# Performance work log

Measured on AMD Instinct MI355X. Metric: run time of the kernel, lower is better.

The kernel has to match this reference:

```python
import jax, jax.numpy as jnp
import numpy as np

HID = 64      # hidden_dim
HEADS = 4     # attention heads
CH = HID // HEADS  # 16 per-head channels
EDIM = 6      # edge_dim
NEG = 0.2     # leaky_relu negative slope


def _glorot(key, shape):
    fan_in, fan_out = shape[0], shape[-1]
    s = np.sqrt(6.0 / (fan_in + fan_out)).astype(np.float32)
    return jax.random.uniform(key, shape, jnp.float32, -s, s)


def setup_inputs() -> dict:
    key = jax.random.key(0)
    ks = iter(jax.random.split(key, 48))
    N, E, T = 100000, 1200000, 20000
    inp = {
        "x": jax.random.normal(next(ks), (N, 7), jnp.float32),
        "pos": jax.random.normal(next(ks), (N, 3), jnp.float32),
        "node_type": jax.random.randint(next(ks), (N,), 0, 2),
        "edge_index": jax.random.randint(next(ks), (2, E), 0, N),
        "edge_attr": jax.random.normal(next(ks), (E, EDIM), jnp.float32),
        "num_tracks": T,
        "hidden_state": jax.random.normal(next(ks), (T, HID), jnp.float32),
        # params
        "type_emb": jax.random.normal(next(ks), (2, 8), jnp.float32),
        "enc_W1": _glorot(next(ks), (18, HID)), "enc_b1": jnp.zeros((HID,), jnp.float32),
        "enc_W2": _glorot(next(ks), (HID, HID)), "enc_b2": jnp.zeros((HID,), jnp.float32),
        "gru_Wi": _glorot(next(ks), (HID, 3 * HID)), "gru_bi": jnp.zeros((3 * HID,), jnp.float32),
        "gru_Wh": _glorot(next(ks), (HID, 3 * HID)), "gru_bh": jnp.zeros((3 * HID,), jnp.float32),
        "dec_W1": _glorot(next(ks), (HID, HID)), "dec_b1": jnp.zeros((HID,), jnp.float32),
        "dec_W2": _glorot(next(ks), (HID, 7)), "dec_b2": jnp.zeros((7,), jnp.float32),
    }
    for g in ("g1", "g2"):
        inp[g + "_Wl"] = _glorot(next(ks), (HID, HID))
        inp[g + "_bl"] = jnp.zeros((HID,), jnp.float32)
        inp[g + "_Wr"] = _glorot(next(ks), (HID, HID))
        inp[g + "_br"] = jnp.zeros((HID,), jnp.float32)
        inp[g + "_We"] = _glorot(next(ks), (EDIM, HID))
        inp[g + "_att"] = _glorot(next(ks), (HEADS, CH))
        inp[g + "_bias"] = jnp.zeros((HID,), jnp.float32)
    return inp


def _segment_softmax(e, seg, n):
    m = jax.ops.segment_max(e, seg, num_segments=n)
    m = jnp.where(jnp.isfinite(m), m, 0.0)
    ex = jnp.exp(e - m[seg])
    s = jax.ops.segment_sum(ex, seg, num_segments=n)
    return ex / (s[seg] + 1e-16)


def _gatv2(h, src, dst, eattr, Wl, bl, Wr, br, We, att, bias):
    N = h.shape[0]
    xl = (h @ Wl + bl).reshape(N, HEADS, CH)
    xr = (h @ Wr + br).reshape(N, HEADS, CH)
    ea = (eattr @ We).reshape(-1, HEADS, CH)
    g = jax.nn.leaky_relu(xl[src] + xr[dst] + ea, NEG)      # [E, H, C]
    e = jnp.einsum('ehc,hc->eh', g, att)                     # [E, H]
    alpha = _segment_softmax(e, dst, N)                      # [E, H]
    msg = xl[src] * alpha[..., None]                         # [E, H, C]
    out = jax.ops.segment_sum(msg, dst, num_segments=N)
    return out.reshape(N, HID) + bias, alpha


def reference(x, pos, node_type, edge_index, edge_attr, num_tracks, hidden_state,
              type_emb, enc_W1, enc_b1, enc_W2, enc_b2,
              g1_Wl, g1_bl, g1_Wr, g1_br, g1_We, g1_att, g1_bias,
              g2_Wl, g2_bl, g2_Wr, g2_br, g2_We, g2_att, g2_bias,
              gru_Wi, gru_bi, gru_Wh, gru_bh,
              dec_W1, dec_b1, dec_W2, dec_b2):
    N = x.shape[0]
    h = jnp.concatenate([x, pos, type_emb[node_type]], axis=-1)
    h = jax.nn.relu(h @ enc_W1 + enc_b1) @ enc_W2 + enc_b2

    # PyG GATv2Conv: add self loops, edge_attr fill_value='mean' (mean of incoming edges)
    src, dst = edge_index[0], edge_index[1]
    deg = jax.ops.segment_sum(jnp.ones(src.shape[0], jnp.float32), dst, num_segments=N)
    loop_attr = jax.ops.segment_sum(edge_attr, dst, num_segments=N) / jnp.maximum(deg, 1.0)[:, None]
    ar = jnp.arange(N)
    src_a = jnp.concatenate([src, ar])
    dst_a = jnp.concatenate([dst, ar])
    eattr_a = jnp.concatenate([edge_attr, loop_attr], axis=0)

    h1, a1 = _gatv2(h, src_a, dst_a, eattr_a, g1_Wl, g1_bl, g1_Wr, g1_br, g1_We, g1_att, g1_bias)
    h1 = jax.nn.relu(h1)
    h2, a2 = _gatv2(h1, src_a, dst_a, eattr_a, g2_Wl, g2_bl, g2_Wr, g2_br, g2_We, g2_att, g2_bias)

    # GRUCell on the first num_tracks nodes
    ht = h2[:num_tracks]
    gi = ht @ gru_Wi + gru_bi
    gh = hidden_state @ gru_Wh + gru_bh
    r = jax.nn.sigmoid(gi[:, :HID] + gh[:, :HID])
    z = jax.nn.sigmoid(gi[:, HID:2 * HID] + gh[:, HID:2 * HID])
    n = jnp.tanh(gi[:, 2 * HID:] + r * gh[:, 2 * HID:])
    new_tracks = (1.0 - z) * n + z * hidden_state

    new_full = jnp.concatenate([new_tracks, h2[num_tracks:]], axis=0)
    out = jax.nn.relu(new_full @ dec_W1 + dec_b1) @ dec_W2 + dec_b2  # [N, 7]
    final = out.at[:, :3].set(pos + out[:, :3])
    final = final.at[:, 3:6].set(x[:, :3] + out[:, 3:6])
    return final, new_full, a1, a2
```

## Files before the change

kernel.cpp:

```cpp
#include <hip/hip_runtime.h>

#define NEG 0.2f
#define SCHUNK 1024
typedef unsigned short u16;

__device__ __forceinline__ float sigmoidf_(float v){ return 1.f/(1.f+__expf(-v)); }
__device__ __forceinline__ int rfl_(int v){ return __builtin_amdgcn_readfirstlane(v); }
__device__ __forceinline__ float bf2f_(unsigned u){ return __uint_as_float(u<<16); }
__device__ __forceinline__ u16 f2bf_(float f){
  unsigned u = __float_as_uint(f);
  u += 0x7FFFu + ((u>>16)&1u);
  return (u16)(u>>16);
}
template<int C>
__device__ __forceinline__ float dppadd_(float p){
  int r = __builtin_amdgcn_update_dpp(0, __float_as_int(p), C, 0xF, 0xF, true);
  return p + __int_as_float(r);
}
__device__ __forceinline__ float dppsum16_(float p){
  p = dppadd_<0x121>(p);
  p = dppadd_<0x122>(p);
  p = dppadd_<0x124>(p);
  p = dppadd_<0x128>(p);
  return p;
}

__global__ __launch_bounds__(256) void enc_kernel(
    const float* __restrict__ x, const float* __restrict__ pos,
    const int* __restrict__ ntype, const float* __restrict__ temb,
    const float* __restrict__ W1, const float* __restrict__ b1,
    const float* __restrict__ W2, const float* __restrict__ b2,
    float* __restrict__ hout, int N)
{
  __shared__ float sW1[18*64];
  __shared__ float sW2[4096];
  __shared__ float fT[4][8*20];
  __shared__ float tT[4][8*64];
  for (int i=threadIdx.x; i<18*64; i+=256) sW1[i]=W1[i];
  for (int i=threadIdx.x; i<4096; i+=256)  sW2[i]=W2[i];
  __syncthreads();
  int lane = threadIdx.x & 63;
  int wid  = threadIdx.x >> 6;
  int n0 = (blockIdx.x*4 + wid)*8;
  if (n0 >= N) return;
  float b1v=b1[lane], b2v=b2[lane];
  #pragma unroll
  for (int m=0;m<8;m++){
    int n=n0+m; float fv=0.f;
    if (n<N){
      if (lane<7)       fv=x[(size_t)n*7+lane];
      else if (lane<10) fv=pos[(size_t)n*3+lane-7];
      else if (lane<18) fv=temb[ntype[n]*8+lane-10];
    }
    if (lane<20) fT[wid][m*20+lane]=fv;
  }
  float t[8];
  #pragma unroll
  for (int m=0;m<8;m++) t[m]=b1v;
  #pragma unroll 2
  for (int k=0;k<18;k++){
    float w=sW1[k*64+lane];
    #pragma unroll
    for (int m=0;m<8;m++) t[m] += fT[wid][m*20+k]*w;
  }
  #pragma unroll
  for (int m=0;m<8;m++){ t[m]=fmaxf(t[m],0.f); tT[wid][m*64+lane]=t[m]; }
  float o[8];
  #pragma unroll
  for (int m=0;m<8;m++) o[m]=b2v;
  #pragma unroll 2
  for (int k=0;k<64;k++){
    float w=sW2[k*64+lane];
    #pragma unroll
    for (int m=0;m<8;m++) o[m] += tT[wid][m*64+k]*w;
  }
  #pragma unroll
  for (int m=0;m<8;m++){ int n=n0+m; if (n<N) hout[(size_t)n*64+lane]=o[m]; }
}

__global__ void deg_kernel(const int* __restrict__ ei, int* __restrict__ deg, int E)
{
  int e = blockIdx.x*256 + threadIdx.x;
  if (e>=E) return;
  atomicAdd(deg + ei[E+e], 1);
}

__global__ __launch_bounds__(256) void scan_reduce(const int* __restrict__ deg, int* __restrict__ bsum, int N)
{
  int base = blockIdx.x*SCHUNK + threadIdx.x*4;
  int s=0;
  #pragma unroll
  for (int j=0;j<4;j++){ int i=base+j; s += (i<N)? deg[i]+1 : 0; }
  #pragma unroll
  for (int d=1;d<64;d<<=1) s += __shfl_xor(s,d);
  __shared__ int ws[4];
  if ((threadIdx.x&63)==0) ws[threadIdx.x>>6]=s;
  __syncthreads();
  if (threadIdx.x==0) bsum[blockIdx.x]=ws[0]+ws[1]+ws[2]+ws[3];
}

__global__ __launch_bounds__(1024) void scan_bsums(const int* __restrict__ bsum, int* __restrict__ bscan, int NB)
{
  int tid = threadIdx.x;
  int lane = tid&63, w = tid>>6;
  int v = (tid<NB)? bsum[tid] : 0;
  int inc = v;
  #pragma unroll
  for (int d=1;d<64;d<<=1){ int t=__shfl_up(inc,d); if (lane>=d) inc+=t; }
  __shared__ int wsum[16], woff[16];
  if (lane==63) wsum[w]=inc;
  __syncthreads();
  if (w==0){
    int s=(lane<16)?wsum[lane]:0; int sc=s;
    #pragma unroll
    for (int d=1;d<16;d<<=1){ int t=__shfl_up(sc,d); if (lane>=d) sc+=t; }
    if (lane<16) woff[lane]=sc-s;
  }
  __syncthreads();
  int excl = woff[w] + inc - v;
  if (tid<NB) bscan[tid]=excl;
}

__global__ __launch_bounds__(256) void scan_final(const int* __restrict__ deg, const int* __restrict__ bscan,
                                                  int* __restrict__ offs, int N)
{
  int lane = threadIdx.x&63, w = threadIdx.x>>6;
  int base = blockIdx.x*SCHUNK + threadIdx.x*4;
  int v[4]; int s=0;
  #pragma unroll
  for (int j=0;j<4;j++){ int i=base+j; v[j]=(i<N)?deg[i]+1:0; s+=v[j]; }
  int inc=s;
  #pragma unroll
  for (int d=1;d<64;d<<=1){ int t=__shfl_up(inc,d); if (lane>=d) inc+=t; }
  __shared__ int wsum[4], woff[4];
  if (lane==63) wsum[w]=inc;
  __syncthreads();
  if (threadIdx.x==0){ woff[0]=0; woff[1]=wsum[0]; woff[2]=wsum[0]+wsum[1]; woff[3]=wsum[0]+wsum[1]+wsum[2]; }
  __syncthreads();
  int excl = bscan[blockIdx.x] + woff[w] + (inc - s);
  #pragma unroll
  for (int j=0;j<4;j++){ int i=base+j; if (i<N) offs[i]=excl; excl+=v[j]; }
}

__global__ void fill_kernel(const int* __restrict__ ei, const int* __restrict__ offs,
                            int* __restrict__ cursor, int2* __restrict__ csr2, int E)
{
  int e = blockIdx.x*256 + threadIdx.x;
  if (e >= E) return;
  int dst = ei[E + e];
  int p = atomicAdd(cursor + dst, 1);
  csr2[offs[dst] + p] = make_int2(e, ei[e]);
}

__global__ __launch_bounds__(256) void xfrm_kernel(
    const float* __restrict__ hin,
    const float* __restrict__ Wl, const float* __restrict__ bl,
    const float* __restrict__ Wr, const float* __restrict__ br,
    u16* __restrict__ xlo, u16* __restrict__ xro, int N)
{
  __shared__ float sWl[4096], sWr[4096];
  __shared__ float hT[4][16*64];
  for (int i=threadIdx.x;i<4096;i+=256){ sWl[i]=Wl[i]; sWr[i]=Wr[i]; }
  __syncthreads();
  int lane=threadIdx.x&63;
  int wid=threadIdx.x>>6;
  int n0=(blockIdx.x*4+wid)*16;
  if (n0>=N) return;
  #pragma unroll
  for (int m=0;m<16;m++){
    int n=n0+m;
    hT[wid][m*64+lane] = (n<N)? hin[(size_t)n*64+lane] : 0.f;
  }
  float blv=bl[lane], brv=br[lane];
  float al[16], ar[16];
  #pragma unroll
  for (int m=0;m<16;m++){ al[m]=blv; ar[m]=brv; }
  #pragma unroll 2
  for (int k=0;k<64;k++){
    float wl=sWl[k*64+lane], wr=sWr[k*64+lane];
    #pragma unroll
    for (int m=0;m<16;m++){
      float hb = hT[wid][m*64+k];
      al[m]+=hb*wl; ar[m]+=hb*wr;
    }
  }
  #pragma unroll
  for (int m=0;m<16;m++){
    int n=n0+m;
    if (n<N){ xlo[(((unsigned)n)<<6)+lane]=f2bf_(al[m]); xro[(((unsigned)n)<<6)+lane]=f2bf_(ar[m]); }
  }
}

#define EDGE_STEP(EIDX, EADD, XV) do {                                       \
    float s_ = (XV) + xrv + (EADD);                                          \
    s_ = fmaxf(s_, NEG*s_);                                                  \
    float p_ = dppsum16_(s_*attv);                                           \
    if (isbase) aout[(((unsigned)(EIDX))<<2)+h] = p_;                        \
    if (__all(p_ <= mmax)) {                                                 \
      float w_ = __expf(p_ - mmax);                                          \
      ssum += w_; acc += w_*(XV);                                            \
    } else {                                                                 \
      float mn_ = fmaxf(mmax, p_);                                           \
      float sc_ = __expf(mmax - mn_);                                        \
      float w_  = __expf(p_ - mn_);                                          \
      ssum = ssum*sc_ + w_;                                                  \
      acc  = acc*sc_ + w_*(XV);                                              \
      mmax = mn_;                                                            \
    }                                                                        \
  } while(0)

#define EDGE_PRE(J) \
    int e##J = rfl_(c##J.x), s##J = rfl_(c##J.y); \
    const float2* q##J = (const float2*)(eattr + (unsigned)e##J*6u); \
    float2 A##J=q##J[0], B##J=q##J[1], C##J=q##J[2]; \
    unsigned xv##J = xlb[(((unsigned)s##J)<<6)+lane];

#define EDGE_BODY(J) \
    float d##J = A##J.x*we0 + A##J.y*we1 + B##J.x*we2 + B##J.y*we3 + C##J.x*we4 + C##J.y*we5; \
    dsum += d##J; \
    EDGE_STEP(e##J, d##J, bf2f_(xv##J));

__global__ __launch_bounds__(256) void gat_kernel(
    const int2* __restrict__ csr2, const int* __restrict__ offs, const int* __restrict__ deg,
    const float* __restrict__ eattr,
    const u16* __restrict__ xlb, const u16* __restrict__ xrb,
    const float* __restrict__ We, const float* __restrict__ att,
    const float* __restrict__ bias,
    float* __restrict__ aout, float2* __restrict__ msbuf,
    float* __restrict__ hout,
    int E, int N, int do_relu)
{
  int lane = threadIdx.x & 63;
  int n = blockIdx.x*4 + (threadIdx.x>>6);
  if (n >= N) return;
  float we0=We[lane], we1=We[64+lane], we2=We[128+lane],
        we3=We[192+lane], we4=We[256+lane], we5=We[320+lane];
  float attv = att[lane];
  float bv = bias[lane];
  float xrv = bf2f_(xrb[(((unsigned)n)<<6)+lane]);
  int h = lane >> 4;
  bool isbase = (lane & 15) == 0;
  int o0 = rfl_(offs[n]);
  int dg = rfl_(deg[n]);
  int oend = o0 + dg;
  float mmax = -3.402823e38f, ssum=0.f, acc=0.f, dsum=0.f;
  int o = o0;
  for (; o+8 <= oend; o += 8){
    int2 c0=csr2[o],   c1=csr2[o+1], c2=csr2[o+2], c3=csr2[o+3],
         c4=csr2[o+4], c5=csr2[o+5], c6=csr2[o+6], c7=csr2[o+7];
    EDGE_PRE(0); EDGE_PRE(1); EDGE_PRE(2); EDGE_PRE(3);
    EDGE_PRE(4); EDGE_PRE(5); EDGE_PRE(6); EDGE_PRE(7);
    EDGE_BODY(0); EDGE_BODY(1); EDGE_BODY(2); EDGE_BODY(3);
    EDGE_BODY(4); EDGE_BODY(5); EDGE_BODY(6); EDGE_BODY(7);
  }
  for (; o+4 <= oend; o += 4){
    int2 c0=csr2[o], c1=csr2[o+1], c2=csr2[o+2], c3=csr2[o+3];
    EDGE_PRE(0); EDGE_PRE(1); EDGE_PRE(2); EDGE_PRE(3);
    EDGE_BODY(0); EDGE_BODY(1); EDGE_BODY(2); EDGE_BODY(3);
  }
  for (; o < oend; ++o){
    int2 c0=csr2[o];
    EDGE_PRE(0);
    EDGE_BODY(0);
  }
  {
    float dS = dsum * (1.f/fmaxf((float)dg,1.f));
    float xvS = bf2f_((unsigned)xlb[(((unsigned)n)<<6)+lane]);
    EDGE_STEP(E+n, dS, xvS);
  }
  float sinv = 1.f/(ssum + 1e-16f);
  if (isbase) msbuf[(((unsigned)n)<<2)+h] = make_float2(mmax, sinv);
  float outv = acc*sinv + bv;
  if (do_relu) outv = fmaxf(outv, 0.f);
  hout[(((unsigned)n)<<6)+lane] = outv;
}

__global__ void alpha_kernel(const int* __restrict__ ei,
                             const float2* __restrict__ ms1, const float2* __restrict__ ms2,
                             float4* __restrict__ a1, float4* __restrict__ a2, int E, int N)
{
  int e = blockIdx.x*256 + threadIdx.x;
  if (e >= E+N) return;
  int dst = (e<E)? ei[E+e] : (e-E);
  {
    float4 r = a1[e];
    const float2* mp = ms1 + (((unsigned)dst)<<2);
    float2 m0=mp[0], m1=mp[1], m2=mp[2], m3=mp[3];
    float4 o;
    o.x = __expf(r.x - m0.x)*m0.y;
    o.y = __expf(r.y - m1.x)*m1.y;
    o.z = __expf(r.z - m2.x)*m2.y;
    o.w = __expf(r.w - m3.x)*m3.y;
    a1[e] = o;
  }
  {
    float4 r = a2[e];
    const float2* mp = ms2 + (((unsigned)dst)<<2);
    float2 m0=mp[0], m1=mp[1], m2=mp[2], m3=mp[3];
    float4 o;
    o.x = __expf(r.x - m0.x)*m0.y;
    o.y = __expf(r.y - m1.x)*m1.y;
    o.z = __expf(r.z - m2.x)*m2.y;
    o.w = __expf(r.w - m3.x)*m3.y;
    a2[e] = o;
  }
}

__global__ __launch_bounds__(256) void grudec_kernel(
    const float* __restrict__ h2, const float* __restrict__ hid,
    const float* __restrict__ Wi, const float* __restrict__ bi,
    const float* __restrict__ Wh, const float* __restrict__ bh,
    const int* __restrict__ Tptr,
    const float* __restrict__ W1, const float* __restrict__ b1,
    const float* __restrict__ W2, const float* __restrict__ b2,
    const float* __restrict__ x, const float* __restrict__ pos,
    float* __restrict__ nf, float* __restrict__ fout, int N)
{
  __shared__ float sW1[4096];
  __shared__ float sW2[448];
  __shared__ float sb2[8];
  __shared__ float tT[4][8*68];
  __shared__ float pT[4][8*68];
  for (int i=threadIdx.x;i<4096;i+=256) sW1[i]=W1[i];
  for (int i=threadIdx.x;i<448;i+=256) sW2[i]=W2[i];
  if (threadIdx.x<7)  sb2[threadIdx.x]=b2[threadIdx.x];
  __syncthreads();
  int lane = threadIdx.x & 63;
  int wid  = threadIdx.x >> 6;
  int n0 = (blockIdx.x*4 + wid)*8;
  if (n0 >= N) return;
  int T = *Tptr;
  float hv[8], nfv[8];
  #pragma unroll
  for (int m=0;m<8;m++){ int n=n0+m; hv[m] = (n<N)? h2[(size_t)n*64+lane] : 0.f; }
  if (n0 < T){
    float pv[8];
    #pragma unroll
    for (int m=0;m<8;m++){ int n=n0+m; pv[m] = (n<T)? hid[(size_t)n*64+lane] : 0.f; }
    #pragma unroll
    for (int m=0;m<8;m++){ tT[wid][m*68+lane]=hv[m]; pT[wid][m*68+lane]=pv[m]; }
    float gr[8],gz[8],gn[8],hr[8],hz[8],hn[8];
    #pragma unroll
    for (int m=0;m<8;m++){ gr[m]=0.f;gz[m]=0.f;gn[m]=0.f;hr[m]=0.f;hz[m]=0.f;hn[m]=0.f; }
    for (int k=0;k<64;k++){
      float wir=Wi[k*192+lane], wiz=Wi[k*192+64+lane], win=Wi[k*192+128+lane];
      float whr=Wh[k*192+lane], whz=Wh[k*192+64+lane], whn=Wh[k*192+128+lane];
      #pragma unroll
      for (int m=0;m<8;m++){
        float a=tT[wid][m*68+k], b=pT[wid][m*68+k];
        gr[m]+=a*wir; gz[m]+=a*wiz; gn[m]+=a*win;
        hr[m]+=b*whr; hz[m]+=b*whz; hn[m]+=b*whn;
      }
    }
    float bir=bi[lane], biz=bi[64+lane], bin=bi[128+lane];
    float bhr=bh[lane], bhz=bh[64+lane], bhn=bh[128+lane];
    #pragma unroll
    for (int m=0;m<8;m++){
      int n=n0+m;
      if (n<T){
        float r  = sigmoidf_(gr[m]+bir + hr[m]+bhr);
        float z  = sigmoidf_(gz[m]+biz + hz[m]+bhz);
        float nn = tanhf(gn[m]+bin + r*(hn[m]+bhn));
        nfv[m] = (1.f-z)*nn + z*pv[m];
      } else {
        nfv[m] = hv[m];
      }
    }
  } else {
    #pragma unroll
    for (int m=0;m<8;m++) nfv[m] = hv[m];
  }
  #pragma unroll
  for (int m=0;m<8;m++){ int n=n0+m; if (n<N) nf[(size_t)n*64+lane]=nfv[m]; }
  #pragma unroll
  for (int m=0;m<8;m++) tT[wid][m*68+lane]=nfv[m];
  float t[8];
  float b1v=b1[lane];
  #pragma unroll
  for (int m=0;m<8;m++) t[m]=b1v;
  #pragma unroll 2
  for (int k=0;k<64;k++){
    float w=sW1[k*64+lane];
    #pragma unroll
    for (int m=0;m<8;m++) t[m] += tT[wid][m*68+k]*w;
  }
  #pragma unroll
  for (int m=0;m<8;m++) t[m]=fmaxf(t[m],0.f);
  #pragma unroll
  for (int m=0;m<8;m++) tT[wid][m*68+lane]=t[m];
  int mm = lane >> 3, cc = lane & 7;
  if (cc < 7){
    float a2 = sb2[cc];
    #pragma unroll 4
    for (int k=0;k<64;k++) a2 += tT[wid][mm*68+k]*sW2[k*7+cc];
    int n = n0+mm;
    if (n < N){
      if (cc<3)      a2 += pos[(size_t)n*3+cc];
      else if (cc<6) a2 += x[(size_t)n*7+(cc-3)];
      fout[(size_t)n*7+cc] = a2;
    }
  }
}

extern "C" void kernel_launch(void* const* d_in, const int* in_sizes, int n_in,
                              void* d_out, int out_size, void* d_ws, size_t ws_size,
                              hipStream_t stream)
{
  const float* x     = (const float*)d_in[0];
  const float* pos   = (const float*)d_in[1];
  const int*   ntype = (const int*)d_in[2];
  const int*   eidx  = (const int*)d_in[3];
  const float* eattr = (const float*)d_in[4];
  const int*   Tptr  = (const int*)d_in[5];
  const float* hid   = (const float*)d_in[6];
  const float* temb  = (const float*)d_in[7];
  const float* encW1 = (const float*)d_in[8];
  const float* encb1 = (const float*)d_in[9];
  const float* encW2 = (const float*)d_in[10];
  const float* encb2 = (const float*)d_in[11];
  const float* gruWi = (const float*)d_in[12];
  const float* grubi = (const float*)d_in[13];
  const float* gruWh = (const float*)d_in[14];
  const float* grubh = (const float*)d_in[15];
  const float* decW1 = (const float*)d_in[16];
  const float* decb1 = (const float*)d_in[17];
  const float* decW2 = (const float*)d_in[18];
  const float* decb2 = (const float*)d_in[19];
  const float* gWl[2]  = {(const float*)d_in[20], (const float*)d_in[27]};
  const float* gbl[2]  = {(const float*)d_in[21], (const float*)d_in[28]};
  const float* gWr[2]  = {(const float*)d_in[22], (const float*)d_in[29]};
  const float* gbr[2]  = {(const float*)d_in[23], (const float*)d_in[30]};
  const float* gWe[2]  = {(const float*)d_in[24], (const float*)d_in[31]};
  const float* gatt[2] = {(const float*)d_in[25], (const float*)d_in[32]};
  const float* gbias[2]= {(const float*)d_in[26], (const float*)d_in[33]};

  int N  = in_sizes[0] / 7;
  int E  = in_sizes[3] / 2;
  int Ea = E + N;
  int NB = (N + SCHUNK - 1) / SCHUNK;

  char* w = (char*)d_ws;
  float* A      = (float*)w; w += (size_t)N*64*sizeof(float);
  float* B      = (float*)w; w += (size_t)N*64*sizeof(float);
  u16*   XL     = (u16*)w;  w += (size_t)N*64*sizeof(u16);
  u16*   XR     = (u16*)w;  w += (size_t)N*64*sizeof(u16);
  int*   deg    = (int*)w;   w += (size_t)N*sizeof(int);
  int*   cursor = (int*)w;   w += (size_t)N*sizeof(int);
  int*   offs   = (int*)w;   w += (size_t)N*sizeof(int);
  int*   bsum   = (int*)w;   w += (size_t)NB*sizeof(int);
  int*   bscan  = (int*)w;   w += (size_t)NB*sizeof(int);
  float2* msbuf1= (float2*)w; w += (size_t)N*4*sizeof(float2);
  float2* msbuf2= (float2*)w; w += (size_t)N*4*sizeof(float2);
  int2*  csr2   = (int2*)w;  w += (size_t)Ea*sizeof(int2);

  float* out_final = (float*)d_out;
  float* out_nf    = out_final + (size_t)N*7;
  float* out_a1    = out_nf + (size_t)N*64;
  float* out_a2    = out_a1 + (size_t)Ea*4;

  hipMemsetAsync(deg, 0, (size_t)2*N*sizeof(int), stream);

  enc_kernel<<<(N+31)/32, 256, 0, stream>>>(x,pos,ntype,temb,encW1,encb1,encW2,encb2,A,N);
  deg_kernel<<<(E+255)/256, 256, 0, stream>>>(eidx, deg, E);
  scan_reduce<<<NB, 256, 0, stream>>>(deg, bsum, N);
  scan_bsums<<<1, 1024, 0, stream>>>(bsum, bscan, NB);
  scan_final<<<NB, 256, 0, stream>>>(deg, bscan, offs, N);
  fill_kernel<<<(E+255)/256, 256, 0, stream>>>(eidx, offs, cursor, csr2, E);

  xfrm_kernel<<<(N+63)/64, 256, 0, stream>>>(A, gWl[0], gbl[0], gWr[0], gbr[0], XL, XR, N);
  gat_kernel<<<(N+3)/4, 256, 0, stream>>>(csr2, offs, deg, eattr, XL, XR,
      gWe[0], gatt[0], gbias[0], out_a1, msbuf1, B, E, N, 1);

  xfrm_kernel<<<(N+63)/64, 256, 0, stream>>>(B, gWl[1], gbl[1], gWr[1], gbr[1], XL, XR, N);
  gat_kernel<<<(N+3)/4, 256, 0, stream>>>(csr2, offs, deg, eattr, XL, XR,
      gWe[1], gatt[1], gbias[1], out_a2, msbuf2, A, E, N, 0);

  alpha_kernel<<<(Ea+255)/256, 256, 0, stream>>>(eidx, msbuf1, msbuf2,
      (float4*)out_a1, (float4*)out_a2, E, N);

  grudec_kernel<<<(N+31)/32, 256, 0, stream>>>(A, hid, gruWi, grubi, gruWh, grubh, Tptr,
      decW1, decb1, decW2, decb2, x, pos, out_nf, out_final, N);
}
```

Baseline: 570.8 us.

## Fuse independent kernels and replace three-pass scan with atomic offset allocation

Horizontally fuses independent work into single launches: encoder with degree counting, the first transform with CSR fill, and GRU/decoder with the alpha normalization. The three-kernel prefix scan becomes one kernel where each block claims its range through an atomic counter. Self-loops are no longer stored in the CSR buffer, and the 8-wide unrolled edge loop in the GAT kernel is removed. The aim is fewer launches and grid drains; the cost is that CSR segment order now depends on atomic timing, and each edge step exposes less memory-level parallelism.

```diff
diff --git a/kernel.cpp b/kernel.cpp
--- a/kernel.cpp
+++ b/kernel.cpp
@@ -1,7 +1,6 @@
 #include <hip/hip_runtime.h>
 
 #define NEG 0.2f
-#define SCHUNK 1024
 typedef unsigned short u16;
 
 __device__ __forceinline__ float sigmoidf_(float v){ return 1.f/(1.f+__expf(-v)); }
@@ -25,17 +24,24 @@
   return p;
 }
 
-__global__ __launch_bounds__(256) void enc_kernel(
+__global__ __launch_bounds__(256) void encdeg_kernel(
     const float* __restrict__ x, const float* __restrict__ pos,
     const int* __restrict__ ntype, const float* __restrict__ temb,
     const float* __restrict__ W1, const float* __restrict__ b1,
     const float* __restrict__ W2, const float* __restrict__ b2,
-    float* __restrict__ hout, int N)
+    float* __restrict__ hout,
+    const int* __restrict__ ei, int* __restrict__ deg,
+    int encB, int E, int N)
 {
   __shared__ float sW1[18*64];
   __shared__ float sW2[4096];
   __shared__ float fT[4][8*20];
   __shared__ float tT[4][8*64];
+  if ((int)blockIdx.x >= encB){
+    int e = ((int)blockIdx.x - encB)*256 + threadIdx.x;
+    if (e < E) atomicAdd(deg + ei[E+e], 1);
+    return;
+  }
   for (int i=threadIdx.x; i<18*64; i+=256) sW1[i]=W1[i];
   for (int i=threadIdx.x; i<4096; i+=256)  sW2[i]=W2[i];
   __syncthreads();
@@ -78,78 +84,79 @@
   for (int m=0;m<8;m++){ int n=n0+m; if (n<N) hout[(size_t)n*64+lane]=o[m]; }
 }
 
-__global__ void deg_kernel(const int* __restrict__ ei, int* __restrict__ deg, int E)
-{
-  int e = blockIdx.x*256 + threadIdx.x;
-  if (e>=E) return;
-  atomicAdd(deg + ei[E+e], 1);
-}
-
-__global__ __launch_bounds__(256) void scan_reduce(const int* __restrict__ deg, int* __restrict__ bsum, int N)
-{
-  int base = blockIdx.x*SCHUNK + threadIdx.x*4;
-  int s=0;
-  #pragma unroll
-  for (int j=0;j<4;j++){ int i=base+j; s += (i<N)? deg[i]+1 : 0; }
-  #pragma unroll
-  for (int d=1;d<64;d<<=1) s += __shfl_xor(s,d);
-  __shared__ int ws[4];
-  if ((threadIdx.x&63)==0) ws[threadIdx.x>>6]=s;
-  __syncthreads();
-  if (threadIdx.x==0) bsum[blockIdx.x]=ws[0]+ws[1]+ws[2]+ws[3];
-}
-
-__global__ __launch_bounds__(1024) void scan_bsums(const int* __restrict__ bsum, int* __restrict__ bscan, int NB)
-{
-  int tid = threadIdx.x;
-  int lane = tid&63, w = tid>>6;
-  int v = (tid<NB)? bsum[tid] : 0;
-  int inc = v;
+__global__ __launch_bounds__(256) void alloc_kernel(
+    const int* __restrict__ deg, int* __restrict__ offs, int* __restrict__ counter, int N)
+{
+  __shared__ int wsum[4], woff[4], sbase;
+  int lane = threadIdx.x & 63, w = threadIdx.x >> 6;
+  int base = blockIdx.x*1024 + threadIdx.x*4;
+  int v[4]; int s=0;
+  #pragma unroll
+  for (int j=0;j<4;j++){ int i=base+j; v[j]=(i<N)?deg[i]:0; s+=v[j]; }
+  int inc=s;
   #pragma unroll
   for (int d=1;d<64;d<<=1){ int t=__shfl_up(inc,d); if (lane>=d) inc+=t; }
-  __shared__ int wsum[16], woff[16];
   if (lane==63) wsum[w]=inc;
   __syncthreads();
-  if (w==0){
-    int s=(lane<16)?wsum[lane]:0; int sc=s;
-    #pragma unroll
-    for (int d=1;d<16;d<<=1){ int t=__shfl_up(sc,d); if (lane>=d) sc+=t; }
-    if (lane<16) woff[lane]=sc-s;
-  }
-  __syncthreads();
-  int excl = woff[w] + inc - v;
-  if (tid<NB) bscan[tid]=excl;
-}
-
-__global__ __launch_bounds__(256) void scan_final(const int* __restrict__ deg, const int* __restrict__ bscan,
-                                                  int* __restrict__ offs, int N)
-{
-  int lane = threadIdx.x&63, w = threadIdx.x>>6;
-  int base = blockIdx.x*SCHUNK + threadIdx.x*4;
-  int v[4]; int s=0;
-  #pragma unroll
-  for (int j=0;j<4;j++){ int i=base+j; v[j]=(i<N)?deg[i]+1:0; s+=v[j]; }
-  int inc=s;
-  #pragma unroll
-  for (int d=1;d<64;d<<=1){ int t=__shfl_up(inc,d); if (lane>=d) inc+=t; }
-  __shared__ int wsum[4], woff[4];
-  if (lane==63) wsum[w]=inc;
-  __syncthreads();
-  if (threadIdx.x==0){ woff[0]=0; woff[1]=wsum[0]; woff[2]=wsum[0]+wsum[1]; woff[3]=wsum[0]+wsum[1]+wsum[2]; }
-  __syncthreads();
-  int excl = bscan[blockIdx.x] + woff[w] + (inc - s);
+  if (threadIdx.x==0){
+    woff[0]=0; woff[1]=wsum[0]; woff[2]=wsum[0]+wsum[1]; woff[3]=wsum[0]+wsum[1]+wsum[2];
+    sbase = atomicAdd(counter, woff[3]+wsum[3]);
+  }
+  __syncthreads();
+  int excl = sbase + woff[w] + (inc - s);
   #pragma unroll
   for (int j=0;j<4;j++){ int i=base+j; if (i<N) offs[i]=excl; excl+=v[j]; }
 }
 
-__global__ void fill_kernel(const int* __restrict__ ei, const int* __restrict__ offs,
-                            int* __restrict__ cursor, int2* __restrict__ csr2, int E)
-{
-  int e = blockIdx.x*256 + threadIdx.x;
-  if (e >= E) return;
-  int dst = ei[E + e];
-  int p = atomicAdd(cursor + dst, 1);
-  csr2[offs[dst] + p] = make_int2(e, ei[e]);
+__global__ __launch_bounds__(256) void xfrmfill_kernel(
+    const float* __restrict__ hin,
+    const float* __restrict__ Wl, const float* __restrict__ bl,
+    const float* __restrict__ Wr, const float* __restrict__ br,
+    u16* __restrict__ xlo, u16* __restrict__ xro,
+    const int* __restrict__ ei, const int* __restrict__ offs,
+    int* __restrict__ cursor, int2* __restrict__ csr2,
+    int xfB, int E, int N)
+{
+  __shared__ float sWl[4096], sWr[4096];
+  __shared__ float hT[4][16*64];
+  if ((int)blockIdx.x >= xfB){
+    int e = ((int)blockIdx.x - xfB)*256 + threadIdx.x;
+    if (e < E){
+      int dst = ei[E + e];
+      int p = atomicAdd(cursor + dst, 1);
+      csr2[offs[dst] + p] = make_int2(e, ei[e]);
+    }
+    return;
+  }
+  for (int i=threadIdx.x;i<4096;i+=256){ sWl[i]=Wl[i]; sWr[i]=Wr[i]; }
+  __syncthreads();
+  int lane=threadIdx.x&63;
+  int wid=threadIdx.x>>6;
+  int n0=(blockIdx.x*4+wid)*16;
+  if (n0>=N) return;
+  #pragma unroll
+  for (int m=0;m<16;m++){
+    int n=n0+m;
+    hT[wid][m*64+lane] = (n<N)? hin[(size_t)n*64+lane] : 0.f;
+  }
+  float blv=bl[lane], brv=br[lane];
+  float al[16], ar[16];
+  #pragma unroll
+  for (int m=0;m<16;m++){ al[m]=blv; ar[m]=brv; }
+  #pragma unroll 2
+  for (int k=0;k<64;k++){
+    float wl=sWl[k*64+lane], wr=sWr[k*64+lane];
+    #pragma unroll
+    for (int m=0;m<16;m++){
+      float hb = hT[wid][m*64+k];
+      al[m]+=hb*wl; ar[m]+=hb*wr;
+    }
+  }
+  #pragma unroll
+  for (int m=0;m<16;m++){
+    int n=n0+m;
+    if (n<N){ xlo[(((unsigned)n)<<6)+lane]=f2bf_(al[m]); xro[(((unsigned)n)<<6)+lane]=f2bf_(ar[m]); }
+  }
 }
 
 __global__ __launch_bounds__(256) void xfrm_kernel(
@@ -245,14 +252,6 @@
   int oend = o0 + dg;
   float mmax = -3.402823e38f, ssum=0.f, acc=0.f, dsum=0.f;
   int o = o0;
-  for (; o+8 <= oend; o += 8){
-    int2 c0=csr2[o],   c1=csr2[o+1], c2=csr2[o+2], c3=csr2[o+3],
-         c4=csr2[o+4], c5=csr2[o+5], c6=csr2[o+6], c7=csr2[o+7];
-    EDGE_PRE(0); EDGE_PRE(1); EDGE_PRE(2); EDGE_PRE(3);
-    EDGE_PRE(4); EDGE_PRE(5); EDGE_PRE(6); EDGE_PRE(7);
-    EDGE_BODY(0); EDGE_BODY(1); EDGE_BODY(2); EDGE_BODY(3);
-    EDGE_BODY(4); EDGE_BODY(5); EDGE_BODY(6); EDGE_BODY(7);
-  }
   for (; o+4 <= oend; o += 4){
     int2 c0=csr2[o], c1=csr2[o+1], c2=csr2[o+2], c3=csr2[o+3];
     EDGE_PRE(0); EDGE_PRE(1); EDGE_PRE(2); EDGE_PRE(3);
@@ -275,38 +274,7 @@
   hout[(((unsigned)n)<<6)+lane] = outv;
 }
 
-__global__ void alpha_kernel(const int* __restrict__ ei,
-                             const float2* __restrict__ ms1, const float2* __restrict__ ms2,
-                             float4* __restrict__ a1, float4* __restrict__ a2, int E, int N)
-{
-  int e = blockIdx.x*256 + threadIdx.x;
-  if (e >= E+N) return;
-  int dst = (e<E)? ei[E+e] : (e-E);
-  {
-    float4 r = a1[e];
-    const float2* mp = ms1 + (((unsigned)dst)<<2);
-    float2 m0=mp[0], m1=mp[1], m2=mp[2], m3=mp[3];
-    float4 o;
-    o.x = __expf(r.x - m0.x)*m0.y;
-    o.y = __expf(r.y - m1.x)*m1.y;
-    o.z = __expf(r.z - m2.x)*m2.y;
-    o.w = __expf(r.w - m3.x)*m3.y;
-    a1[e] = o;
-  }
-  {
-    float4 r = a2[e];
-    const float2* mp = ms2 + (((unsigned)dst)<<2);
-    float2 m0=mp[0], m1=mp[1], m2=mp[2], m3=mp[3];
-    float4 o;
-    o.x = __expf(r.x - m0.x)*m0.y;
-    o.y = __expf(r.y - m1.x)*m1.y;
-    o.z = __expf(r.z - m2.x)*m2.y;
-    o.w = __expf(r.w - m3.x)*m3.y;
-    a2[e] = o;
-  }
-}
-
-__global__ __launch_bounds__(256) void grudec_kernel(
+__global__ __launch_bounds__(256) void grudecalpha_kernel(
     const float* __restrict__ h2, const float* __restrict__ hid,
     const float* __restrict__ Wi, const float* __restrict__ bi,
     const float* __restrict__ Wh, const float* __restrict__ bh,
@@ -314,13 +282,46 @@
     const float* __restrict__ W1, const float* __restrict__ b1,
     const float* __restrict__ W2, const float* __restrict__ b2,
     const float* __restrict__ x, const float* __restrict__ pos,
-    float* __restrict__ nf, float* __restrict__ fout, int N)
+    float* __restrict__ nf, float* __restrict__ fout,
+    const int* __restrict__ ei,
+    const float2* __restrict__ ms1, const float2* __restrict__ ms2,
+    float4* __restrict__ a1, float4* __restrict__ a2,
+    int gdB, int E, int N)
 {
   __shared__ float sW1[4096];
   __shared__ float sW2[448];
   __shared__ float sb2[8];
   __shared__ float tT[4][8*68];
   __shared__ float pT[4][8*68];
+  if ((int)blockIdx.x >= gdB){
+    int e = ((int)blockIdx.x - gdB)*256 + threadIdx.x;
+    if (e < E+N){
+      int dst = (e<E)? ei[E+e] : (e-E);
+      {
+        float4 r = a1[e];
+        const float2* mp = ms1 + (((unsigned)dst)<<2);
+        float2 m0=mp[0], m1=mp[1], m2=mp[2], m3=mp[3];
+        float4 o;
+        o.x = __expf(r.x - m0.x)*m0.y;
+        o.y = __expf(r.y - m1.x)*m1.y;
+        o.z = __expf(r.z - m2.x)*m2.y;
+        o.w = __expf(r.w - m3.x)*m3.y;
+        a1[e] = o;
+      }
+      {
+        float4 r = a2[e];
+        const float2* mp = ms2 + (((unsigned)dst)<<2);
+        float2 m0=mp[0], m1=mp[1], m2=mp[2], m3=mp[3];
+        float4 o;
+        o.x = __expf(r.x - m0.x)*m0.y;
+        o.y = __expf(r.y - m1.x)*m1.y;
+        o.z = __expf(r.z - m2.x)*m2.y;
+        o.w = __expf(r.w - m3.x)*m3.y;
+        a2[e] = o;
+      }
+    }
+    return;
+  }
   for (int i=threadIdx.x;i<4096;i+=256) sW1[i]=W1[i];
   for (int i=threadIdx.x;i<448;i+=256) sW2[i]=W2[i];
   if (threadIdx.x<7)  sb2[threadIdx.x]=b2[threadIdx.x];
@@ -390,14 +391,14 @@
   for (int m=0;m<8;m++) tT[wid][m*68+lane]=t[m];
   int mm = lane >> 3, cc = lane & 7;
   if (cc < 7){
-    float a2 = sb2[cc];
+    float a2v = sb2[cc];
     #pragma unroll 4
-    for (int k=0;k<64;k++) a2 += tT[wid][mm*68+k]*sW2[k*7+cc];
+    for (int k=0;k<64;k++) a2v += tT[wid][mm*68+k]*sW2[k*7+cc];
     int n = n0+mm;
     if (n < N){
-      if (cc<3)      a2 += pos[(size_t)n*3+cc];
-      else if (cc<6) a2 += x[(size_t)n*7+(cc-3)];
-      fout[(size_t)n*7+cc] = a2;
+      if (cc<3)      a2v += pos[(size_t)n*3+cc];
+      else if (cc<6) a2v += x[(size_t)n*7+(cc-3)];
+      fout[(size_t)n*7+cc] = a2v;
     }
   }
 }
@@ -437,7 +438,6 @@
   int N  = in_sizes[0] / 7;
   int E  = in_sizes[3] / 2;
   int Ea = E + N;
-  int NB = (N + SCHUNK - 1) / SCHUNK;
 
   char* w = (char*)d_ws;
   float* A      = (float*)w; w += (size_t)N*64*sizeof(float);
@@ -446,38 +446,41 @@
   u16*   XR     = (u16*)w;  w += (size_t)N*64*sizeof(u16);
   int*   deg    = (int*)w;   w += (size_t)N*sizeof(int);
   int*   cursor = (int*)w;   w += (size_t)N*sizeof(int);
+  int*   counter= (int*)w;   w += 4*sizeof(int);
   int*   offs   = (int*)w;   w += (size_t)N*sizeof(int);
-  int*   bsum   = (int*)w;   w += (size_t)NB*sizeof(int);
-  int*   bscan  = (int*)w;   w += (size_t)NB*sizeof(int);
   float2* msbuf1= (float2*)w; w += (size_t)N*4*sizeof(float2);
   float2* msbuf2= (float2*)w; w += (size_t)N*4*sizeof(float2);
-  int2*  csr2   = (int2*)w;  w += (size_t)Ea*sizeof(int2);
+  int2*  csr2   = (int2*)w;  w += (size_t)E*sizeof(int2);
 
   float* out_final = (float*)d_out;
   float* out_nf    = out_final + (size_t)N*7;
   float* out_a1    = out_nf + (size_t)N*64;
   float* out_a2    = out_a1 + (size_t)Ea*4;
 
-  hipMemsetAsync(deg, 0, (size_t)2*N*sizeof(int), stream);
-
-  enc_kernel<<<(N+31)/32, 256, 0, stream>>>(x,pos,ntype,temb,encW1,encb1,encW2,encb2,A,N);
-  deg_kernel<<<(E+255)/256, 256, 0, stream>>>(eidx, deg, E);
-  scan_reduce<<<NB, 256, 0, stream>>>(deg, bsum, N);
-  scan_bsums<<<1, 1024, 0, stream>>>(bsum, bscan, NB);
-  scan_final<<<NB, 256, 0, stream>>>(deg, bscan, offs, N);
-  fill_kernel<<<(E+255)/256, 256, 0, stream>>>(eidx, offs, cursor, csr2, E);
-
-  xfrm_kernel<<<(N+63)/64, 256, 0, stream>>>(A, gWl[0], gbl[0], gWr[0], gbr[0], XL, XR, N);
+  hipMemsetAsync(deg, 0, ((size_t)2*N + 4)*sizeof(int), stream);
+
+  int encB = (N+31)/32;
+  int degB = (E+255)/256;
+  encdeg_kernel<<<encB+degB, 256, 0, stream>>>(x,pos,ntype,temb,encW1,encb1,encW2,encb2,A,
+      eidx, deg, encB, E, N);
+
+  alloc_kernel<<<(N+1023)/1024, 256, 0, stream>>>(deg, offs, counter, N);
+
+  int xfB = (N+63)/64;
+  int flB = (E+255)/256;
+  xfrmfill_kernel<<<xfB+flB, 256, 0, stream>>>(A, gWl[0], gbl[0], gWr[0], gbr[0], XL, XR,
+      eidx, offs, cursor, csr2, xfB, E, N);
+
   gat_kernel<<<(N+3)/4, 256, 0, stream>>>(csr2, offs, deg, eattr, XL, XR,
       gWe[0], gatt[0], gbias[0], out_a1, msbuf1, B, E, N, 1);
 
-  xfrm_kernel<<<(N+63)/64, 256, 0, stream>>>(B, gWl[1], gbl[1], gWr[1], gbr[1], XL, XR, N);
+  xfrm_kernel<<<xfB, 256, 0, stream>>>(B, gWl[1], gbl[1], gWr[1], gbr[1], XL, XR, N);
   gat_kernel<<<(N+3)/4, 256, 0, stream>>>(csr2, offs, deg, eattr, XL, XR,
       gWe[1], gatt[1], gbias[1], out_a2, msbuf2, A, E, N, 0);
 
-  alpha_kernel<<<(Ea+255)/256, 256, 0, stream>>>(eidx, msbuf1, msbuf2,
-      (float4*)out_a1, (float4*)out_a2, E, N);
-
-  grudec_kernel<<<(N+31)/32, 256, 0, stream>>>(A, hid, gruWi, grubi, gruWh, grubh, Tptr,
-      decW1, decb1, decW2, decb2, x, pos, out_nf, out_final, N);
-}
+  int gdB = (N+31)/32;
+  int alB = (Ea+255)/256;
+  grudecalpha_kernel<<<gdB+alB, 256, 0, stream>>>(A, hid, gruWi, grubi, gruWh, grubh, Tptr,
+      decW1, decb1, decW2, decb2, x, pos, out_nf, out_final,
+      eidx, msbuf1, msbuf2, (float4*)out_a1, (float4*)out_a2, gdB, E, N);
+}
```

Measured after the change: 567.8 us. Within noise of the previous version (-0.5%).
